# Optimization experiments

Measured on AMD Instinct MI355X. Metric: run time of the kernel, lower is better.

Reference implementation:

```python
import jax, jax.numpy as jnp
import numpy as np

B = 65536      # batch size
H = 256        # hidden_size (args['hid_dim'])
MID = 300      # hard-coded encoder bottleneck in CommonFeatureExtractor
THR = 0.6      # similarity_threshold


def _lin(k, fin, fout):
    return jax.random.normal(k, (fin, fout), jnp.float32) / np.sqrt(fin)


def setup_inputs() -> dict:
    key = jax.random.key(0)
    ks = jax.random.split(key, 24)
    inp = {
        'brics': jax.random.normal(ks[0], (B, H), jnp.float32),
        'function_group': jax.random.normal(ks[1], (B, H), jnp.float32),
        'pharmacophore': jax.random.normal(ks[2], (B, H), jnp.float32),
    }
    # three fp encoders: Linear(H,300) -> ReLU -> (Dropout eval) -> Linear(300,H)
    for n, (k1, k2) in zip(['b', 'f', 'p'], [(ks[3], ks[4]), (ks[5], ks[6]), (ks[7], ks[8])]):
        inp['W1_' + n] = _lin(k1, H, MID)
        inp['b1_' + n] = jnp.zeros((MID,), jnp.float32)
        inp['W2_' + n] = _lin(k2, MID, H)
        inp['b2_' + n] = jnp.zeros((H,), jnp.float32)
    inp['Wg'] = _lin(ks[9], 3 * H, 3)        # weight_generator
    inp['bg_v'] = jnp.zeros((3,), jnp.float32)
    inp['We'] = _lin(ks[10], H, H)           # enhancement_layer
    inp['be_v'] = jnp.zeros((H,), jnp.float32)
    inp['Wf'] = _lin(ks[11], 2 * H, H)       # fusion_layer
    inp['bf_v'] = jnp.zeros((H,), jnp.float32)
    return inp


def _fwd(brics, function_group, pharmacophore,
         W1_b, b1_b, W2_b, b2_b, W1_f, b1_f, W2_f, b2_f, W1_p, b1_p, W2_p, b2_p,
         Wg, bg_v, We, be_v, Wf, bf_v):
    def enc(x, W1, b1, W2, b2):
        return jax.nn.relu(x @ W1 + b1) @ W2 + b2  # dropout in eval mode = identity

    eb = enc(brics, W1_b, b1_b, W2_b, b2_b)
    ef = enc(function_group, W1_f, b1_f, W2_f, b2_f)
    ep = enc(pharmacophore, W1_p, b1_p, W2_p, b2_p)

    fps = jnp.stack([eb, ef, ep], axis=1)                              # [B,3,H]
    fpn = fps / jnp.maximum(jnp.linalg.norm(fps, axis=-1, keepdims=True), 1e-12)

    # the 3 unordered pairs (0,1),(0,2),(1,2); the torch sort is irrelevant
    # because the selected pairs are combined by a permutation-invariant
    # softmax-weighted sum.
    ii = jnp.array([0, 0, 1])
    jj = jnp.array([1, 2, 2])
    elem = fpn[:, ii] * fpn[:, jj]                                     # [B,3,H]
    sims = elem.sum(-1)                                                # [B,3] cosine sims
    pmask = sims > THR
    common = 0.5 * (fps[:, ii] + fps[:, jj]) * (elem > THR)            # [B,3,H]

    has = pmask.any(-1)                                                # [B]
    m = jnp.max(jnp.where(pmask, sims, -jnp.inf), axis=-1, keepdims=True)
    m = jnp.where(jnp.isfinite(m), m, 0.0)
    e = jnp.where(pmask, jnp.exp(sims - m), 0.0)                       # masked softmax
    w = e / jnp.maximum(e.sum(-1, keepdims=True), 1e-12)
    sample_common = (common * w[..., None]).sum(1)                     # [B,H]
    common_features = jnp.where(has[:, None], sample_common, fps.mean(1))

    allc = jnp.concatenate([eb, ef, ep], axis=1)                       # [B,3H]
    fw = jax.nn.softmax(allc @ Wg + bg_v, axis=1)                      # [B,3]
    weighted = eb * fw[:, 0:1] + ef * fw[:, 1:2] + ep * fw[:, 2:3]

    enh = jax.nn.sigmoid(common_features @ We + be_v)
    fused = jnp.concatenate([weighted, common_features * enh], axis=1) @ Wf + bf_v
    return fused


def reference(brics, function_group, pharmacophore,
              W1_b, b1_b, W2_b, b2_b, W1_f, b1_f, W2_f, b2_f, W1_p, b1_p, W2_p, b2_p,
              Wg, bg_v, We, be_v, Wf, bf_v):
    return _fwd(brics, function_group, pharmacophore,
                W1_b, b1_b, W2_b, b2_b, W1_f, b1_f, W2_f, b2_f, W1_p, b1_p, W2_p, b2_p,
                Wg, bg_v, We, be_v, Wf, bf_v)
```

## Files before the change

kernel.cpp:

```cpp
#include <hip/hip_runtime.h>

typedef unsigned short u16;
typedef __bf16 bf16x8 __attribute__((ext_vector_type(8)));
typedef float f32x4 __attribute__((ext_vector_type(4)));
typedef unsigned short u16x8 __attribute__((ext_vector_type(8)));

__device__ __forceinline__ float b2f(u16 b){ union{unsigned u; float f;} v; v.u=((unsigned)b)<<16; return v.f; }
__device__ __forceinline__ u16 f2b(float f){ unsigned u=__builtin_bit_cast(unsigned,f); return (u16)((u+0x7fffu+((u>>16)&1u))>>16); }
__device__ __forceinline__ float wred32(float v){
  #pragma unroll
  for(int off=16; off>0; off>>=1) v += __shfl_xor(v, off, 64);
  return v;
}
__device__ __forceinline__ void stOut(u16* p, float v){ *p = f2b(v); }
__device__ __forceinline__ void stOut(float* p, float v){ *p = v; }

__device__ __forceinline__ void gload_lds16(const void* g, void* l){
  __builtin_amdgcn_global_load_lds(
      (const __attribute__((address_space(1))) void*)g,
      (__attribute__((address_space(3))) void*)l, 16, 0, 0);
}

__device__ __forceinline__ void stageA8(u16* dst, const float* src){
  float4 a = *(const float4*)src;
  float4 b = *(const float4*)(src+4);
  ushort4 o0; o0.x=f2b(a.x); o0.y=f2b(a.y); o0.z=f2b(a.z); o0.w=f2b(a.w);
  ushort4 o1; o1.x=f2b(b.x); o1.y=f2b(b.y); o1.z=f2b(b.z); o1.w=f2b(b.w);
  *(ushort4*)dst = o0;
  *(ushort4*)(dst+4) = o1;
}

struct GP {
  const void* A[3];
  const void* A2;
  const u16*  Wt[3];
  const float* bias[3];
  void* C[3];
  const u16* mult;
  int lda, K, Nreal, ldc, ldm;
};

template<int MODE, typename OT, typename AT, bool DUAL>
__global__ __launch_bounds__(256) void gemm_k(GP p)
{
  const int z = blockIdx.z;
  const AT* __restrict__ A  = (const AT*)p.A[z];
  const AT* __restrict__ A2 = (const AT*)p.A2;
  const u16* __restrict__ Wt = p.Wt[z];
  const float* __restrict__ bias = p.bias[z];
  OT* __restrict__ C = (OT*)p.C[z];
  const int lda = p.lda, K = p.K, Nreal = p.Nreal, ldc = p.ldc, ldm = p.ldm;

  __shared__ __align__(16) u16 As[128*64];
  __shared__ __align__(16) u16 Bs[64*64];
  const int tid = threadIdx.x;
  const size_t m0 = (size_t)blockIdx.x * 128;
  const int n0 = blockIdx.y * 64;
  const int lane = tid & 63, w = tid >> 6;
  const int lr = lane & 15, quad = lane >> 4;
  const int wr = (w >> 1) * 64, wc = (w & 1) * 32;
  const int swz = (lr & 7) << 3;
  const int KH = K >> 1;

  f32x4 acc[4][2];
  #pragma unroll
  for(int i=0;i<4;++i)
    #pragma unroll
    for(int j=0;j<2;++j) acc[i][j] = (f32x4){0.f,0.f,0.f,0.f};

  for(int k0=0; k0<K; k0+=64){
    const AT* Ap = A;
    int kcol = k0;
    if (DUAL && k0 >= KH) { Ap = A2; kcol = k0 - KH; }

    if constexpr (__is_same(AT, u16)) {
      #pragma unroll
      for(int it=0; it<4; ++it){
        int cbase = it*256 + w*64;
        int ch = cbase + lane;
        int r = ch >> 3;
        int ce = ((ch & 7) * 8) ^ ((r & 7) << 3);
        gload_lds16(Ap + (m0+r)*(size_t)lda + kcol + ce, &As[cbase*8]);
      }
    } else {
      #pragma unroll
      for(int it=0; it<4; ++it){
        int ch = tid + 256*it; int r = ch>>3, s = (ch&7)*8;
        stageA8(&As[r*64 + (s ^ ((r&7)<<3))], Ap + (m0+r)*(size_t)lda + kcol + s);
      }
    }
    #pragma unroll
    for(int it=0; it<2; ++it){
      int cbase = it*256 + w*64;
      int ch = cbase + lane;
      int r = ch >> 3;
      int ce = ((ch & 7) * 8) ^ ((r & 7) << 3);
      gload_lds16(Wt + (size_t)(n0+r)*K + k0 + ce, &Bs[cbase*8]);
    }
    __syncthreads();
    #pragma unroll
    for(int kk=0; kk<64; kk+=32){
      bf16x8 af[4], bfr[2];
      #pragma unroll
      for(int i=0;i<4;++i)
        af[i]  = *(const bf16x8*)&As[(wr + i*16 + lr)*64 + ((kk + quad*8) ^ swz)];
      #pragma unroll
      for(int j=0;j<2;++j)
        bfr[j] = *(const bf16x8*)&Bs[(wc + j*16 + lr)*64 + ((kk + quad*8) ^ swz)];
      #pragma unroll
      for(int i=0;i<4;++i)
        #pragma unroll
        for(int j=0;j<2;++j)
          acc[i][j] = __builtin_amdgcn_mfma_f32_16x16x32_bf16(af[i], bfr[j], acc[i][j], 0, 0, 0);
    }
    __syncthreads();
  }
  #pragma unroll
  for(int j=0;j<2;++j){
    int col = n0 + wc + j*16 + lr;
    float bv = (col < Nreal) ? bias[col] : 0.f;
    #pragma unroll
    for(int i=0;i<4;++i){
      #pragma unroll
      for(int r=0;r<4;++r){
        size_t row = m0 + wr + i*16 + quad*4 + r;
        size_t ci = row*(size_t)ldc + col;
        float v = acc[i][j][r] + bv;
        if(MODE==1) v = fmaxf(v, 0.f);
        if(MODE==2){
          float mv = b2f(p.mult[row*(size_t)ldm + col]);
          v = mv * __builtin_amdgcn_rcpf(1.f + __expf(-v));
        }
        stOut(&C[ci], v);
      }
    }
  }
}

struct TPar { const float* src; u16* dst; int K, N, Kp, Np; };
struct TArgs { TPar p[8]; };
__global__ __launch_bounds__(256) void transpose_all(TArgs args){
  TPar p = args.p[blockIdx.y];
  int n = blockIdx.x;
  if (n >= p.Np) return;
  for (int k = threadIdx.x; k < p.Kp; k += 256){
    u16 v = 0;
    if (n < p.N && k < p.K) v = f2b(p.src[(size_t)k*p.N + n]);
    p.dst[(size_t)n*p.Kp + k] = v;
  }
}

__global__ __launch_bounds__(256) void mid_k(
    const u16* eb, const u16* ef, const u16* ep,
    const float* __restrict__ Wg, const float* __restrict__ bg,
    u16* common, u16* weighted)
{
  const int wid = threadIdx.x >> 6, lane = threadIdx.x & 63;
  const int half = lane >> 5, l5 = lane & 31;
  const size_t row = (size_t)blockIdx.x * 8 + wid*2 + half;
  const size_t base = row*256 + l5*8;

  u16x8 vb = *(const u16x8*)(eb + base);
  u16x8 vf = *(const u16x8*)(ef + base);
  u16x8 vp = *(const u16x8*)(ep + base);
  float fb[8], ff[8], fp[8];
  #pragma unroll
  for(int j=0;j<8;++j){ fb[j]=b2f(vb[j]); ff[j]=b2f(vf[j]); fp[j]=b2f(vp[j]); }

  float sb=0, sf=0, sp=0, d01=0, d02=0, d12=0, g0=0, g1=0, g2=0;
  #pragma unroll
  for(int j=0;j<8;++j){
    sb += fb[j]*fb[j]; sf += ff[j]*ff[j]; sp += fp[j]*fp[j];
    d01 += fb[j]*ff[j]; d02 += fb[j]*fp[j]; d12 += ff[j]*fp[j];
  }
  #pragma unroll
  for(int seg=0; seg<3; ++seg){
    const float* x = (seg==0) ? fb : (seg==1) ? ff : fp;
    const float* wg = Wg + ((size_t)seg*256 + l5*8)*3;
    float wv[24];
    #pragma unroll
    for(int q=0;q<6;++q){
      float4 t = *(const float4*)(wg + q*4);
      wv[q*4+0]=t.x; wv[q*4+1]=t.y; wv[q*4+2]=t.z; wv[q*4+3]=t.w;
    }
    #pragma unroll
    for(int j=0;j<8;++j){
      g0 += x[j]*wv[j*3+0];
      g1 += x[j]*wv[j*3+1];
      g2 += x[j]*wv[j*3+2];
    }
  }
  sb=wred32(sb); sf=wred32(sf); sp=wred32(sp);
  d01=wred32(d01); d02=wred32(d02); d12=wred32(d12);
  g0=wred32(g0); g1=wred32(g1); g2=wred32(g2);

  float inb  = __builtin_amdgcn_rsqf(fmaxf(sb, 1e-24f));
  float invf = __builtin_amdgcn_rsqf(fmaxf(sf, 1e-24f));
  float inp  = __builtin_amdgcn_rsqf(fmaxf(sp, 1e-24f));
  float s01 = d01*inb*invf, s02 = d02*inb*inp, s12 = d12*invf*inp;

  g0 += bg[0]; g1 += bg[1]; g2 += bg[2];
  float gm = fmaxf(g0, fmaxf(g1, g2));
  float e0 = __expf(g0-gm), e1 = __expf(g1-gm), e2 = __expf(g2-gm);
  float res = __builtin_amdgcn_rcpf(e0+e1+e2);
  float fw0 = e0*res, fw1 = e1*res, fw2 = e2*res;

  bool p0 = s01 > 0.6f, p1 = s02 > 0.6f, p2 = s12 > 0.6f;
  bool has = p0 || p1 || p2;
  float mm = -__builtin_inff();
  if(p0) mm = fmaxf(mm, s01);
  if(p1) mm = fmaxf(mm, s02);
  if(p2) mm = fmaxf(mm, s12);
  if(!has) mm = 0.f;
  float q0 = p0 ? __expf(s01-mm) : 0.f;
  float q1 = p1 ? __expf(s02-mm) : 0.f;
  float q2 = p2 ? __expf(s12-mm) : 0.f;
  float rqs = __builtin_amdgcn_rcpf(fmaxf(q0+q1+q2, 1e-12f));
  float w0 = q0*rqs, w1 = q1*rqs, w2 = q2*rqs;

  u16x8 oc, ow;
  #pragma unroll
  for(int j=0;j<8;++j){
    float a = fb[j], b = ff[j], c = fp[j];
    float na = a*inb, nbv = b*invf, nc = c*inp;
    float c0 = (na*nbv > 0.6f) ? 0.5f*(a+b) : 0.f;
    float c1 = (na*nc  > 0.6f) ? 0.5f*(a+c) : 0.f;
    float c2 = (nbv*nc > 0.6f) ? 0.5f*(b+c) : 0.f;
    float sc = c0*w0 + c1*w1 + c2*w2;
    float cf = has ? sc : (a+b+c)*(1.f/3.f);
    float wv = a*fw0 + b*fw1 + c*fw2;
    oc[j] = f2b(cf); ow[j] = f2b(wv);
  }
  *(u16x8*)(common + base) = oc;
  *(u16x8*)(weighted + base) = ow;
}

extern "C" void kernel_launch(void* const* d_in, const int* in_sizes, int n_in,
                              void* d_out, int out_size, void* d_ws, size_t ws_size,
                              hipStream_t stream) {
  const float* brics = (const float*)d_in[0];
  const float* fg    = (const float*)d_in[1];
  const float* ph    = (const float*)d_in[2];
  const float* W1[3] = {(const float*)d_in[3], (const float*)d_in[7], (const float*)d_in[11]};
  const float* b1[3] = {(const float*)d_in[4], (const float*)d_in[8], (const float*)d_in[12]};
  const float* W2[3] = {(const float*)d_in[5], (const float*)d_in[9], (const float*)d_in[13]};
  const float* b2[3] = {(const float*)d_in[6], (const float*)d_in[10], (const float*)d_in[14]};
  const float* Wg = (const float*)d_in[15];
  const float* bg = (const float*)d_in[16];
  const float* We = (const float*)d_in[17];
  const float* be = (const float*)d_in[18];
  const float* Wf = (const float*)d_in[19];
  const float* bf = (const float*)d_in[20];
  float* out = (float*)d_out;

  const int M = in_sizes[0] / 256;

  char* wsp = (char*)d_ws;
  size_t off = 0;
  auto carve = [&](size_t elems)->u16* {
    u16* p = (u16*)(wsp + off);
    off += ((elems*sizeof(u16)) + 255) & ~(size_t)255;
    return p;
  };
  u16* xb0 = carve((size_t)M*256);
  u16* xb1 = carve((size_t)M*256);
  u16* xb2 = carve((size_t)M*256);
  u16* Wt1[3], *Wt2[3];
  for(int i=0;i<3;++i) Wt1[i] = carve(320*256);
  for(int i=0;i<3;++i) Wt2[i] = carve(256*320);
  u16* WtE = carve(256*256);
  u16* WtF = carve(256*512);

  size_t hb = (((size_t)M*320*sizeof(u16)) + 255) & ~(size_t)255;
  bool batched = (off + 3*hb) <= ws_size;
  u16* hh[3];
  hh[0] = (u16*)(wsp + off);
  hh[1] = batched ? (u16*)(wsp + off + hb)   : hh[0];
  hh[2] = batched ? (u16*)(wsp + off + 2*hb) : hh[0];
  (void)n_in; (void)out_size;

  TArgs ta;
  for(int i=0;i<3;++i){
    ta.p[i]   = {W1[i], Wt1[i], 256, 300, 256, 320};
    ta.p[3+i] = {W2[i], Wt2[i], 300, 256, 320, 256};
  }
  ta.p[6] = {We, WtE, 256, 256, 256, 256};
  ta.p[7] = {Wf, WtF, 512, 256, 512, 256};
  transpose_all<<<dim3(512, 8), 256, 0, stream>>>(ta);

  const float* xin[3] = {brics, fg, ph};
  u16* encp[3] = {xb0, xb1, xb2};
  if (batched) {
    GP g1{};
    for(int i=0;i<3;++i){ g1.A[i]=xin[i]; g1.Wt[i]=Wt1[i]; g1.bias[i]=b1[i]; g1.C[i]=hh[i]; }
    g1.lda=256; g1.K=256; g1.Nreal=300; g1.ldc=320;
    gemm_k<1,u16,float,false><<<dim3(M/128, 5, 3), 256, 0, stream>>>(g1);
    GP g2{};
    for(int i=0;i<3;++i){ g2.A[i]=hh[i]; g2.Wt[i]=Wt2[i]; g2.bias[i]=b2[i]; g2.C[i]=encp[i]; }
    g2.lda=320; g2.K=320; g2.Nreal=256; g2.ldc=256;
    gemm_k<0,u16,u16,false><<<dim3(M/128, 4, 3), 256, 0, stream>>>(g2);
  } else {
    for(int i=0;i<3;++i){
      GP g1{}; g1.A[0]=xin[i]; g1.Wt[0]=Wt1[i]; g1.bias[0]=b1[i]; g1.C[0]=hh[0];
      g1.lda=256; g1.K=256; g1.Nreal=300; g1.ldc=320;
      gemm_k<1,u16,float,false><<<dim3(M/128, 5, 1), 256, 0, stream>>>(g1);
      GP g2{}; g2.A[0]=hh[0]; g2.Wt[0]=Wt2[i]; g2.bias[0]=b2[i]; g2.C[0]=encp[i];
      g2.lda=320; g2.K=320; g2.Nreal=256; g2.ldc=256;
      gemm_k<0,u16,u16,false><<<dim3(M/128, 4, 1), 256, 0, stream>>>(g2);
    }
  }

  mid_k<<<M/8, 256, 0, stream>>>(xb0, xb1, xb2, Wg, bg, xb2, xb0);

  {
    GP gg{}; gg.A[0]=xb2; gg.Wt[0]=WtE; gg.bias[0]=be; gg.C[0]=xb1;
    gg.mult=xb2; gg.lda=256; gg.K=256; gg.Nreal=256; gg.ldc=256; gg.ldm=256;
    gemm_k<2,u16,u16,false><<<dim3(M/128, 4, 1), 256, 0, stream>>>(gg);
  }

  {
    GP gf{}; gf.A[0]=xb0; gf.A2=xb1; gf.Wt[0]=WtF; gf.bias[0]=bf; gf.C[0]=out;
    gf.lda=256; gf.K=512; gf.Nreal=256; gf.ldc=256;
    gemm_k<0,float,u16,true><<<dim3(M/128, 4, 1), 256, 0, stream>>>(gf);
  }
}
```

Baseline: 530.2 us.

## Use full-width N tiles per block with double-buffered LDS staging

Each GEMM block now uses 512 threads and covers the whole output width (256 or 320 columns), so the A tile is loaded once instead of once per N tile. Global-to-LDS staging is double-buffered: the next K tile is prefetched while MFMAs run on the current one, and fp32 A loads are held in registers and converted after compute. This removes redundant A reads and exposes load latency to overlap. In exchange it uses more LDS and registers per block, which can lower occupancy, and the grid has fewer blocks.

```diff
diff --git a/kernel.cpp b/kernel.cpp
--- a/kernel.cpp
+++ b/kernel.cpp
@@ -21,13 +21,48 @@
       (__attribute__((address_space(3))) void*)l, 16, 0, 0);
 }
 
-__device__ __forceinline__ void stageA8(u16* dst, const float* src){
-  float4 a = *(const float4*)src;
-  float4 b = *(const float4*)(src+4);
-  ushort4 o0; o0.x=f2b(a.x); o0.y=f2b(a.y); o0.z=f2b(a.z); o0.w=f2b(a.w);
-  ushort4 o1; o1.x=f2b(b.x); o1.y=f2b(b.y); o1.z=f2b(b.z); o1.w=f2b(b.w);
-  *(ushort4*)dst = o0;
-  *(ushort4*)(dst+4) = o1;
+template<int PER>
+__device__ __forceinline__ void stage_tile_b16(const u16* __restrict__ base, int rstride,
+                                               int kcol, u16* lds, int w, int lane){
+  #pragma unroll
+  for(int it=0; it<PER; ++it){
+    int cbase = it*512 + w*64;
+    int ch = cbase + lane;
+    int r = ch >> 3;
+    int ce = ((ch & 7) * 8) ^ ((r & 7) << 3);
+    gload_lds16(base + (size_t)r*rstride + kcol + ce, lds + cbase*8);
+  }
+}
+
+struct Af32Regs { float4 a0, b0, a1, b1; };
+__device__ __forceinline__ void loadA_f32(Af32Regs& rg, const float* __restrict__ Ap,
+                                          int lda, int kcol, int tid){
+  {
+    int ch = tid;       int r = ch>>3, s = (ch&7)*8;
+    const float* src = Ap + (size_t)r*lda + kcol + s;
+    rg.a0 = *(const float4*)src; rg.b0 = *(const float4*)(src+4);
+  }
+  {
+    int ch = tid + 512; int r = ch>>3, s = (ch&7)*8;
+    const float* src = Ap + (size_t)r*lda + kcol + s;
+    rg.a1 = *(const float4*)src; rg.b1 = *(const float4*)(src+4);
+  }
+}
+__device__ __forceinline__ void writeA_f32(const Af32Regs& rg, u16* As, int tid){
+  {
+    int ch = tid;       int r = ch>>3, s = (ch&7)*8;
+    u16* dst = &As[r*64 + (s ^ ((r&7)<<3))];
+    ushort4 o0{f2b(rg.a0.x),f2b(rg.a0.y),f2b(rg.a0.z),f2b(rg.a0.w)};
+    ushort4 o1{f2b(rg.b0.x),f2b(rg.b0.y),f2b(rg.b0.z),f2b(rg.b0.w)};
+    *(ushort4*)dst = o0; *(ushort4*)(dst+4) = o1;
+  }
+  {
+    int ch = tid + 512; int r = ch>>3, s = (ch&7)*8;
+    u16* dst = &As[r*64 + (s ^ ((r&7)<<3))];
+    ushort4 o0{f2b(rg.a1.x),f2b(rg.a1.y),f2b(rg.a1.z),f2b(rg.a1.w)};
+    ushort4 o1{f2b(rg.b1.x),f2b(rg.b1.y),f2b(rg.b1.z),f2b(rg.b1.w)};
+    *(ushort4*)dst = o0; *(ushort4*)(dst+4) = o1;
+  }
 }
 
 struct GP {
@@ -40,8 +75,8 @@
   int lda, K, Nreal, ldc, ldm;
 };
 
-template<int MODE, typename OT, typename AT, bool DUAL>
-__global__ __launch_bounds__(256) void gemm_k(GP p)
+template<int MODE, typename OT, typename AT, bool DUAL, int NWT>
+__global__ __launch_bounds__(512, 2) void gemm_w(GP p)
 {
   const int z = blockIdx.z;
   const AT* __restrict__ A  = (const AT*)p.A[z];
@@ -49,76 +84,77 @@
   const u16* __restrict__ Wt = p.Wt[z];
   const float* __restrict__ bias = p.bias[z];
   OT* __restrict__ C = (OT*)p.C[z];
-  const int lda = p.lda, K = p.K, Nreal = p.Nreal, ldc = p.ldc, ldm = p.ldm;
-
-  __shared__ __align__(16) u16 As[128*64];
-  __shared__ __align__(16) u16 Bs[64*64];
+  const int lda = p.lda, K = p.K, ldc = p.ldc;
+
+  __shared__ __align__(16) u16 As[2][128*64];
+  __shared__ __align__(16) u16 Bs[2][NWT*64*64];
+
   const int tid = threadIdx.x;
   const size_t m0 = (size_t)blockIdx.x * 128;
-  const int n0 = blockIdx.y * 64;
   const int lane = tid & 63, w = tid >> 6;
   const int lr = lane & 15, quad = lane >> 4;
-  const int wr = (w >> 1) * 64, wc = (w & 1) * 32;
+  const int wr = (w >> 2) * 64, wc = (w & 3) * (NWT*16);
   const int swz = (lr & 7) << 3;
-  const int KH = K >> 1;
-
-  f32x4 acc[4][2];
+  const int KH = K >> 1, NT = K >> 6;
+
+  f32x4 acc[4][NWT];
   #pragma unroll
   for(int i=0;i<4;++i)
     #pragma unroll
-    for(int j=0;j<2;++j) acc[i][j] = (f32x4){0.f,0.f,0.f,0.f};
-
-  for(int k0=0; k0<K; k0+=64){
-    const AT* Ap = A;
-    int kcol = k0;
-    if (DUAL && k0 >= KH) { Ap = A2; kcol = k0 - KH; }
-
+    for(int j=0;j<NWT;++j) acc[i][j] = (f32x4){0.f,0.f,0.f,0.f};
+
+  const AT* Ab1 = A + m0*(size_t)lda;
+  const AT* Ab2 = DUAL ? (A2 + m0*(size_t)lda) : nullptr;
+
+  {
     if constexpr (__is_same(AT, u16)) {
-      #pragma unroll
-      for(int it=0; it<4; ++it){
-        int cbase = it*256 + w*64;
-        int ch = cbase + lane;
-        int r = ch >> 3;
-        int ce = ((ch & 7) * 8) ^ ((r & 7) << 3);
-        gload_lds16(Ap + (m0+r)*(size_t)lda + kcol + ce, &As[cbase*8]);
-      }
+      stage_tile_b16<2>((const u16*)Ab1, lda, 0, As[0], w, lane);
     } else {
-      #pragma unroll
-      for(int it=0; it<4; ++it){
-        int ch = tid + 256*it; int r = ch>>3, s = (ch&7)*8;
-        stageA8(&As[r*64 + (s ^ ((r&7)<<3))], Ap + (m0+r)*(size_t)lda + kcol + s);
-      }
-    }
-    #pragma unroll
-    for(int it=0; it<2; ++it){
-      int cbase = it*256 + w*64;
-      int ch = cbase + lane;
-      int r = ch >> 3;
-      int ce = ((ch & 7) * 8) ^ ((r & 7) << 3);
-      gload_lds16(Wt + (size_t)(n0+r)*K + k0 + ce, &Bs[cbase*8]);
-    }
-    __syncthreads();
+      Af32Regs rg; loadA_f32(rg, (const float*)Ab1, lda, 0, tid);
+      writeA_f32(rg, As[0], tid);
+    }
+    stage_tile_b16<NWT>(Wt, K, 0, Bs[0], w, lane);
+  }
+  __syncthreads();
+
+  int cur = 0;
+  for(int t=0; t<NT; ++t){
+    const int knext = (t+1) << 6;
+    const bool pf = (t+1) < NT;
+    Af32Regs rg;
+    if (pf){
+      const AT* Ap = Ab1; int kc = knext;
+      if (DUAL && knext >= KH) { Ap = Ab2; kc = knext - KH; }
+      if constexpr (__is_same(AT, u16))
+        stage_tile_b16<2>((const u16*)Ap, lda, kc, As[cur^1], w, lane);
+      else
+        loadA_f32(rg, (const float*)Ap, lda, kc, tid);
+      stage_tile_b16<NWT>(Wt, K, knext, Bs[cur^1], w, lane);
+    }
     #pragma unroll
     for(int kk=0; kk<64; kk+=32){
-      bf16x8 af[4], bfr[2];
+      bf16x8 af[4], bq[NWT];
       #pragma unroll
       for(int i=0;i<4;++i)
-        af[i]  = *(const bf16x8*)&As[(wr + i*16 + lr)*64 + ((kk + quad*8) ^ swz)];
+        af[i] = *(const bf16x8*)&As[cur][(wr + i*16 + lr)*64 + ((kk + quad*8) ^ swz)];
       #pragma unroll
-      for(int j=0;j<2;++j)
-        bfr[j] = *(const bf16x8*)&Bs[(wc + j*16 + lr)*64 + ((kk + quad*8) ^ swz)];
+      for(int j=0;j<NWT;++j)
+        bq[j] = *(const bf16x8*)&Bs[cur][(wc + j*16 + lr)*64 + ((kk + quad*8) ^ swz)];
       #pragma unroll
       for(int i=0;i<4;++i)
         #pragma unroll
-        for(int j=0;j<2;++j)
-          acc[i][j] = __builtin_amdgcn_mfma_f32_16x16x32_bf16(af[i], bfr[j], acc[i][j], 0, 0, 0);
-    }
+        for(int j=0;j<NWT;++j)
+          acc[i][j] = __builtin_amdgcn_mfma_f32_16x16x32_bf16(af[i], bq[j], acc[i][j], 0, 0, 0);
+    }
+    if constexpr (!__is_same(AT, u16)) { if (pf) writeA_f32(rg, As[cur^1], tid); }
     __syncthreads();
-  }
-  #pragma unroll
-  for(int j=0;j<2;++j){
-    int col = n0 + wc + j*16 + lr;
-    float bv = (col < Nreal) ? bias[col] : 0.f;
+    cur ^= 1;
+  }
+
+  #pragma unroll
+  for(int j=0;j<NWT;++j){
+    int col = wc + j*16 + lr;
+    float bv = (col < p.Nreal) ? bias[col] : 0.f;
     #pragma unroll
     for(int i=0;i<4;++i){
       #pragma unroll
@@ -128,7 +164,7 @@
         float v = acc[i][j][r] + bv;
         if(MODE==1) v = fmaxf(v, 0.f);
         if(MODE==2){
-          float mv = b2f(p.mult[row*(size_t)ldm + col]);
+          float mv = b2f(p.mult[row*(size_t)p.ldm + col]);
           v = mv * __builtin_amdgcn_rcpf(1.f + __expf(-v));
         }
         stOut(&C[ci], v);
@@ -294,19 +330,19 @@
     GP g1{};
     for(int i=0;i<3;++i){ g1.A[i]=xin[i]; g1.Wt[i]=Wt1[i]; g1.bias[i]=b1[i]; g1.C[i]=hh[i]; }
     g1.lda=256; g1.K=256; g1.Nreal=300; g1.ldc=320;
-    gemm_k<1,u16,float,false><<<dim3(M/128, 5, 3), 256, 0, stream>>>(g1);
+    gemm_w<1,u16,float,false,5><<<dim3(M/128, 1, 3), 512, 0, stream>>>(g1);
     GP g2{};
     for(int i=0;i<3;++i){ g2.A[i]=hh[i]; g2.Wt[i]=Wt2[i]; g2.bias[i]=b2[i]; g2.C[i]=encp[i]; }
     g2.lda=320; g2.K=320; g2.Nreal=256; g2.ldc=256;
-    gemm_k<0,u16,u16,false><<<dim3(M/128, 4, 3), 256, 0, stream>>>(g2);
+    gemm_w<0,u16,u16,false,4><<<dim3(M/128, 1, 3), 512, 0, stream>>>(g2);
   } else {
     for(int i=0;i<3;++i){
       GP g1{}; g1.A[0]=xin[i]; g1.Wt[0]=Wt1[i]; g1.bias[0]=b1[i]; g1.C[0]=hh[0];
       g1.lda=256; g1.K=256; g1.Nreal=300; g1.ldc=320;
-      gemm_k<1,u16,float,false><<<dim3(M/128, 5, 1), 256, 0, stream>>>(g1);
+      gemm_w<1,u16,float,false,5><<<dim3(M/128, 1, 1), 512, 0, stream>>>(g1);
       GP g2{}; g2.A[0]=hh[0]; g2.Wt[0]=Wt2[i]; g2.bias[0]=b2[i]; g2.C[0]=encp[i];
       g2.lda=320; g2.K=320; g2.Nreal=256; g2.ldc=256;
-      gemm_k<0,u16,u16,false><<<dim3(M/128, 4, 1), 256, 0, stream>>>(g2);
+      gemm_w<0,u16,u16,false,4><<<dim3(M/128, 1, 1), 512, 0, stream>>>(g2);
     }
   }
 
@@ -315,12 +351,12 @@
   {
     GP gg{}; gg.A[0]=xb2; gg.Wt[0]=WtE; gg.bias[0]=be; gg.C[0]=xb1;
     gg.mult=xb2; gg.lda=256; gg.K=256; gg.Nreal=256; gg.ldc=256; gg.ldm=256;
-    gemm_k<2,u16,u16,false><<<dim3(M/128, 4, 1), 256, 0, stream>>>(gg);
+    gemm_w<2,u16,u16,false,4><<<dim3(M/128, 1, 1), 512, 0, stream>>>(gg);
   }
 
   {
     GP gf{}; gf.A[0]=xb0; gf.A2=xb1; gf.Wt[0]=WtF; gf.bias[0]=bf; gf.C[0]=out;
     gf.lda=256; gf.K=512; gf.Nreal=256; gf.ldc=256;
-    gemm_k<0,float,u16,true><<<dim3(M/128, 4, 1), 256, 0, stream>>>(gf);
-  }
-}
+    gemm_w<0,float,u16,true,4><<<dim3(M/128, 1, 1), 512, 0, stream>>>(gf);
+  }
+}
```

Result: faster. 497.5 us (-6.2%).
